# Kernel tuning notes

Measured on AMD Instinct MI355X. Metric: run time of the kernel, lower is better.

## Reference

```python
import jax, jax.numpy as jnp
import numpy as np

B, C, H, W = 4, 256, 64, 64
CQK = C // 8  # 32


def setup_inputs() -> dict:
    key = jax.random.key(0)
    ks = jax.random.split(key, 8)
    s = 0.05
    return {
        "x": jax.random.normal(ks[0], (B, C, H, W), dtype=jnp.float32),
        "wq": jax.random.normal(ks[1], (CQK, C), dtype=jnp.float32) * s,
        "bq": jax.random.normal(ks[2], (CQK,), dtype=jnp.float32) * s,
        "wk": jax.random.normal(ks[3], (CQK, C), dtype=jnp.float32) * s,
        "bk": jax.random.normal(ks[4], (CQK,), dtype=jnp.float32) * s,
        "wv": jax.random.normal(ks[5], (C, C), dtype=jnp.float32) * s,
        "bv": jax.random.normal(ks[6], (C,), dtype=jnp.float32) * s,
        "gamma": jax.random.normal(ks[7], (1,), dtype=jnp.float32),
    }


def reference(x, wq, bq, wk, bk, wv, bv, gamma):
    b, c, h, w = x.shape
    n = h * w
    xf = x.reshape(b, c, n)  # (B, C, N)
    # 1x1 conv + bias + ReLU (Conv2d wrapper default activate='relu')
    q = jax.nn.relu(jnp.einsum('oc,bcn->bon', wq, xf) + bq[:, None])  # (B, CQK, N)
    k = jax.nn.relu(jnp.einsum('oc,bcn->bon', wk, xf) + bk[:, None])  # (B, CQK, N)
    v = jax.nn.relu(jnp.einsum('oc,bcn->bon', wv, xf) + bv[:, None])  # (B, C, N)
    # energy[b, i, j] = sum_c q[b, c, i] * k[b, c, j]
    energy = jnp.einsum('bci,bcj->bij', q, k)  # (B, N, N)
    attention = jax.nn.softmax(energy, axis=-1)
    # out[b, c, i] = sum_j v[b, c, j] * attention[b, i, j]
    out = jnp.einsum('bcj,bij->bci', v, attention)  # (B, C, N)
    out = out.reshape(b, c, h, w)
    return gamma[0] * out + x
```

## Files before the change

### kernel.cpp

```cpp
#include <hip/hip_runtime.h>
#include <stdint.h>


#define NB 4
#define CD 256
#define ND 4096
#define CQ 32
#define LOG2E 1.4426950408889634f

typedef __attribute__((ext_vector_type(4))) float f32x4;
typedef __attribute__((ext_vector_type(8))) _Float16 f16x8;
typedef __attribute__((ext_vector_type(4))) unsigned short u16x4;
typedef __attribute__((ext_vector_type(8))) unsigned short u16x8;
typedef __attribute__((ext_vector_type(2))) unsigned int u32x2;
typedef __attribute__((ext_vector_type(4))) int i32x4;

static __device__ __forceinline__ unsigned short f2h(float f) {
    union { _Float16 h; unsigned short u; } cv; cv.h = (_Float16)f; return cv.u;
}
static __device__ __forceinline__ float fexp2(float xv) {
    float r; asm("v_exp_f32 %0, %1" : "=v"(r) : "v"(xv)); return r;
}

__global__ __launch_bounds__(256) void cvt_kernel(
    const float* __restrict__ x,
    const float* __restrict__ wq, const float* __restrict__ wk,
    const float* __restrict__ wv,
    unsigned short* __restrict__ xh, unsigned short* __restrict__ Wh)
{
    __shared__ unsigned short xt[64 * 72];
    if (blockIdx.x >= 1024) {
        const int idx = (blockIdx.x - 1024) * 256 + threadIdx.x;
        const int m = idx >> 6, kq = (idx & 63) << 2;
        const float* src = (m < 32) ? (wq + (size_t)m * CD + kq)
                         : (m < 64) ? (wk + (size_t)(m - 32) * CD + kq)
                                    : (wv + (size_t)(m - 64) * CD + kq);
        const f32x4 v = *reinterpret_cast<const f32x4*>(src);
        u16x4 h;
#pragma unroll
        for (int u = 0; u < 4; ++u) h[u] = f2h(v[u]);
        *reinterpret_cast<u16x4*>(Wh + (size_t)m * CD + kq) = h;
        return;
    }
    const int t  = threadIdx.x;
    const int nt = blockIdx.x & 63, ct = (blockIdx.x >> 6) & 3, b = blockIdx.x >> 8;
    const int n0 = nt << 6, c0 = ct << 6;

    const float* xb = x + ((size_t)(b * CD + c0)) * ND + n0;
#pragma unroll
    for (int s = t; s < 1024; s += 256) {
        const int c = s >> 4, nq = (s & 15) << 2;
        const f32x4 v = *reinterpret_cast<const f32x4*>(xb + (size_t)c * ND + nq);
        u16x4 h;
#pragma unroll
        for (int u = 0; u < 4; ++u) h[u] = f2h(v[u]);
        *reinterpret_cast<u16x4*>(&xt[c * 72 + nq]) = h;
    }
    __syncthreads();

    const int n = t >> 2, cb = (t & 3) << 4;
    u16x8 o0, o1;
#pragma unroll
    for (int u = 0; u < 8; ++u) o0[u] = xt[(cb + u) * 72 + n];
#pragma unroll
    for (int u = 0; u < 8; ++u) o1[u] = xt[(cb + 8 + u) * 72 + n];
    unsigned short* dst = xh + ((size_t)(b * ND + n0 + n)) * CD + c0 + cb;
    *reinterpret_cast<u16x8*>(dst)     = o0;
    *reinterpret_cast<u16x8*>(dst + 8) = o1;
}

__global__ __launch_bounds__(320) void proj_kernel(
    const unsigned short* __restrict__ Wh, const unsigned short* __restrict__ xh,
    const float* __restrict__ bq, const float* __restrict__ bk,
    const float* __restrict__ bv,
    unsigned short* __restrict__ Qt, unsigned short* __restrict__ Kt,
    unsigned short* __restrict__ Vp)
{
    const int tid = threadIdx.x;
    const int lane = tid & 63;
    const int w = __builtin_amdgcn_readfirstlane(tid >> 6);
    const int m16 = lane & 15, g4 = lane >> 4;
    const int b = blockIdx.x >> 6, n0 = (blockIdx.x & 63) << 6;

    f32x4 acc[4][4];
#pragma unroll
    for (int a = 0; a < 4; ++a)
#pragma unroll
        for (int c = 0; c < 4; ++c) acc[a][c] = (f32x4){0.f, 0.f, 0.f, 0.f};

    const unsigned short* Wrow = Wh + (size_t)(w * 64 + m16) * CD;
    const unsigned short* Xrow = xh + ((size_t)(b * ND + n0 + m16)) * CD;

#pragma unroll
    for (int ks = 0; ks < 8; ++ks) {
        const int ko = ks * 32 + g4 * 8;
        f16x8 af[4], bf[4];
#pragma unroll
        for (int ms = 0; ms < 4; ++ms)
            af[ms] = *reinterpret_cast<const f16x8*>(Wrow + (size_t)ms * 16 * CD + ko);
#pragma unroll
        for (int ns = 0; ns < 4; ++ns)
            bf[ns] = *reinterpret_cast<const f16x8*>(Xrow + (size_t)ns * 16 * CD + ko);
        if (w == 0) {
#pragma unroll
            for (int ms = 0; ms < 4; ++ms)
#pragma unroll
                for (int ns = 0; ns < 4; ++ns)
                    acc[ms][ns] = __builtin_amdgcn_mfma_f32_16x16x32_f16(
                        af[ms], bf[ns], acc[ms][ns], 0, 0, 0);
        } else {
#pragma unroll
            for (int ms = 0; ms < 4; ++ms)
#pragma unroll
                for (int ns = 0; ns < 4; ++ns)
                    acc[ms][ns] = __builtin_amdgcn_mfma_f32_16x16x32_f16(
                        bf[ns], af[ms], acc[ms][ns], 0, 0, 0);
        }
    }

    if (w == 0) {
#pragma unroll
        for (int ms = 0; ms < 4; ++ms) {
            const int seg = ms * 16;
            const int mb  = seg + g4 * 4;
            const f32x4 bias = (seg < 32) ? *reinterpret_cast<const f32x4*>(bq + mb)
                                          : *reinterpret_cast<const f32x4*>(bk + (mb - 32));
#pragma unroll
            for (int ns = 0; ns < 4; ++ns) {
                const int n = n0 + ns * 16 + m16;
                u16x4 h;
                if (seg < 32) {
#pragma unroll
                    for (int r = 0; r < 4; ++r)
                        h[r] = f2h(fmaxf(acc[ms][ns][r] + bias[r], 0.f) * LOG2E);
                    *reinterpret_cast<u16x4*>(Qt + ((size_t)(b * ND + n)) * CQ + mb) = h;
                } else {
#pragma unroll
                    for (int r = 0; r < 4; ++r)
                        h[r] = f2h(fmaxf(acc[ms][ns][r] + bias[r], 0.f));
                    *reinterpret_cast<u16x4*>(Kt + ((size_t)(b * ND + n)) * CQ + (mb - 32)) = h;
                }
            }
        }
    } else {
        const int cbase = (w - 1) * 64;
#pragma unroll
        for (int ms = 0; ms < 4; ++ms) {
            const int c = cbase + ms * 16 + m16;
            const float bval = bv[c];
#pragma unroll
            for (int ns = 0; ns < 4; ++ns) {
                const int n = n0 + ns * 16 + g4 * 4;
                u16x4 h;
#pragma unroll
                for (int r = 0; r < 4; ++r)
                    h[r] = f2h(fmaxf(acc[ms][ns][r] + bval, 0.f));
                unsigned short* dst = Vp
                    + ((size_t)((b * 128 + (n >> 5)) * 16 + (c >> 4))) * 512
                    + ((((n >> 3) & 3) * 16 + (c & 15)) * 8) + (n & 7);
                *reinterpret_cast<u16x4*>(dst) = h;
            }
        }
    }
}

__global__ __launch_bounds__(512, 2) void attn_kernel(
    const unsigned short* __restrict__ Qt, const unsigned short* __restrict__ Kt,
    const unsigned short* __restrict__ Vp, const float* __restrict__ x,
    const float* __restrict__ gamma, float* __restrict__ out)
{
    __shared__ __align__(16) unsigned char smem[68096];
    __shared__ int gctr[2];
    float* scales = reinterpret_cast<float*>(smem + 32768);
    int*   flags  = reinterpret_cast<int*>(smem + 34816);
    float* Ocomb  = reinterpret_cast<float*>(smem);
    float* mfin   = reinterpret_cast<float*>(smem + 66560);
    float* lfin   = reinterpret_cast<float*>(smem + 67072);
    float* wfac   = reinterpret_cast<float*>(smem + 67584);

    const int tid  = threadIdx.x;
    const int lane = tid & 63;
    const int w8   = __builtin_amdgcn_readfirstlane(tid >> 6);
    const int g    = w8 >> 2;
    const int ws   = w8 & 3;
    const int m16  = lane & 15;
    const int g4   = lane >> 4;
    const int wg   = (blockIdx.x & 7) * 32 + (blockIdx.x >> 3);
    const int b    = wg >> 6;
    const int i0   = (wg & 63) << 6;

    if (tid < 2) gctr[tid] = 0;
    __syncthreads();

    const f16x8 qfrag = *reinterpret_cast<const f16x8*>(
        Qt + ((size_t)(b * ND + i0 + ws * 16 + m16)) * CQ + g4 * 8);
    const unsigned short* kb = Kt + ((size_t)(b * ND + m16)) * CQ + g4 * 8;
    const unsigned short* vpc =
        Vp + ((size_t)(b * 128 * 16 + ws * 4)) * 512 + lane * 8;

    f32x4 oacc[4][4];
#pragma unroll
    for (int a = 0; a < 4; ++a)
#pragma unroll
        for (int c = 0; c < 4; ++c) oacc[a][c] = (f32x4){0.f, 0.f, 0.f, 0.f};
    float mrow = -1e30f;
    float lrow = 0.f;
    const f32x4 zero4 = {0.f, 0.f, 0.f, 0.f};

    const int jbase = g * 2048;
    const int irow  = ws * 16 + m16;
    const int iswz  = (m16 & 7) << 4;

    auto LOADK = [&](f16x8 (&kr)[4], int j) {
#pragma unroll
        for (int t = 0; t < 4; ++t)
            kr[t] = *reinterpret_cast<const f16x8*>(kb + (size_t)(j + t * 16) * CQ);
    };

    auto GSYNC = [&](int k) {
        asm volatile("s_waitcnt lgkmcnt(0)" ::: "memory");
        if (lane == 0) atomicAdd(&gctr[g], 1);
        const int tgt = (k + 1) * 4;
        int cv;
        do {
            __builtin_amdgcn_s_sleep(1);
            cv = __builtin_amdgcn_readfirstlane(*(volatile int*)&gctr[g]);
        } while (cv < tgt);
    };

    auto STEP = [&](int k, f16x8 (&kc)[4], f16x8 (&kn)[4]) {
        const int j0  = jbase + k * 64;
        const int par = k & 1;
        unsigned char* pb = smem + g * 16384 + par * 8192;

        const int jblk0 = j0 >> 5;
        f16x8 vf[2][4];
#pragma unroll
        for (int jh = 0; jh < 2; ++jh)
#pragma unroll
            for (int cs = 0; cs < 4; ++cs)
                vf[jh][cs] = *reinterpret_cast<const f16x8*>(
                    vpc + (size_t)((jblk0 + jh) * 16 + cs) * 512);
        const int jn = (k < 31) ? (j0 + 64) : jbase;
        LOADK(kn, jn);

        f32x4 s[4];
#pragma unroll
        for (int t = 0; t < 4; ++t)
            s[t] = __builtin_amdgcn_mfma_f32_16x16x32_f16(kc[t], qfrag, zero4, 0, 0, 0);

        float pm = s[0][0];
#pragma unroll
        for (int t = 0; t < 4; ++t)
#pragma unroll
            for (int r = 0; r < 4; ++r) pm = fmaxf(pm, s[t][r]);
        float sc = 1.0f;
        int myresc = 0;
        if (__ballot(pm <= mrow + 8.0f) != ~0ull) {
            float pr = fmaxf(pm, __shfl_xor(pm, 16));
            pr = fmaxf(pr, __shfl_xor(pr, 32));
            const float mnew = fmaxf(mrow, pr);
            sc = fexp2(mrow - mnew);
            mrow = mnew;
            myresc = 1;
        }
        float rs = 0.f;
#pragma unroll
        for (int t = 0; t < 4; ++t)
#pragma unroll
            for (int r = 0; r < 4; ++r) { s[t][r] = fexp2(s[t][r] - mrow); rs += s[t][r]; }
        lrow = lrow * sc + rs;

#pragma unroll
        for (int t = 0; t < 4; ++t) {
            u32x2 pw;
            pw[0] = __builtin_bit_cast(unsigned int,
                        __builtin_amdgcn_cvt_pkrtz(s[t][0], s[t][1]));
            pw[1] = __builtin_bit_cast(unsigned int,
                        __builtin_amdgcn_cvt_pkrtz(s[t][2], s[t][3]));
            const int lo = (irow * 128 + t * 32 + g4 * 8) ^ iswz;
            *reinterpret_cast<u32x2*>(pb + lo) = pw;
        }
        if (g4 == 0)   scales[(g * 2 + par) * 64 + irow] = sc;
        if (lane == 0) flags[(g * 2 + par) * 4 + ws] = myresc;

        GSYNC(k);

        const i32x4 fl = *reinterpret_cast<const i32x4*>(flags + (g * 2 + par) * 4);
        const int anyresc = __builtin_amdgcn_readfirstlane(fl[0] | fl[1] | fl[2] | fl[3]);
        if (anyresc) {
#pragma unroll
            for (int is = 0; is < 4; ++is) {
                const f32x4 sr = *reinterpret_cast<const f32x4*>(
                    scales + (g * 2 + par) * 64 + is * 16 + g4 * 4);
#pragma unroll
                for (int r = 0; r < 4; ++r)
#pragma unroll
                    for (int cs = 0; cs < 4; ++cs) oacc[is][cs][r] *= sr[r];
            }
        }

        __builtin_amdgcn_s_setprio(1);
#pragma unroll
        for (int jh = 0; jh < 2; ++jh) {
#pragma unroll
            for (int is = 0; is < 4; ++is) {
                const int lo = ((is * 16 + m16) * 128 + jh * 64 + g4 * 16) ^ iswz;
                const f16x8 pf = *reinterpret_cast<const f16x8*>(pb + lo);
#pragma unroll
                for (int cs = 0; cs < 4; ++cs)
                    oacc[is][cs] = __builtin_amdgcn_mfma_f32_16x16x32_f16(
                        pf, vf[jh][cs], oacc[is][cs], 0, 0, 0);
            }
        }
        __builtin_amdgcn_s_setprio(0);
    };

    f16x8 kA[4], kB[4];
    LOADK(kA, jbase);

#pragma unroll 1
    for (int k2 = 0; k2 < 16; ++k2) {
        STEP(2 * k2,     kA, kB);
        STEP(2 * k2 + 1, kB, kA);
    }

    lrow += __shfl_xor(lrow, 16);
    lrow += __shfl_xor(lrow, 32);
    if (g4 == 0) { mfin[g * 64 + irow] = mrow; lfin[g * 64 + irow] = lrow; }
    __syncthreads();

    if (tid < 128) {
        const int gg = tid >> 6, i = tid & 63;
        const float m0 = mfin[i], m1 = mfin[64 + i];
        const float M  = fmaxf(m0, m1);
        const float e0 = fexp2(m0 - M), e1 = fexp2(m1 - M);
        const float den = lfin[i] * e0 + lfin[64 + i] * e1;
        wfac[gg * 64 + i] = ((gg == 0) ? e0 : e1) / den;
    }
    __syncthreads();

    if (g == 0) {
#pragma unroll
        for (int is = 0; is < 4; ++is) {
            const f32x4 f = *reinterpret_cast<const f32x4*>(wfac + is * 16 + g4 * 4);
#pragma unroll
            for (int cs = 0; cs < 4; ++cs)
#pragma unroll
                for (int r = 0; r < 4; ++r)
                    Ocomb[(is * 16 + g4 * 4 + r) * 260 + ws * 64 + cs * 16 + m16] =
                        oacc[is][cs][r] * f[r];
        }
    }
    __syncthreads();
    if (g == 1) {
#pragma unroll
        for (int is = 0; is < 4; ++is) {
            const f32x4 f = *reinterpret_cast<const f32x4*>(wfac + 64 + is * 16 + g4 * 4);
#pragma unroll
            for (int cs = 0; cs < 4; ++cs)
#pragma unroll
                for (int r = 0; r < 4; ++r)
                    Ocomb[(is * 16 + g4 * 4 + r) * 260 + ws * 64 + cs * 16 + m16] +=
                        oacc[is][cs][r] * f[r];
        }
    }
    __syncthreads();

    const float gm = gamma[0];
#pragma unroll
    for (int pass = 0; pass < 8; ++pass) {
        const int c  = (tid >> 4) + pass * 32;
        const int ib = (tid & 15) * 4;
        f32x4 o;
#pragma unroll
        for (int u = 0; u < 4; ++u) o[u] = Ocomb[(ib + u) * 260 + c];
        const size_t idx = ((size_t)(b * CD + c)) * ND + i0 + ib;
        const f32x4 xv = *reinterpret_cast<const f32x4*>(x + idx);
        f32x4 res;
#pragma unroll
        for (int u = 0; u < 4; ++u) res[u] = gm * o[u] + xv[u];
        *reinterpret_cast<f32x4*>(out + idx) = res;
    }
}

extern "C" void kernel_launch(void* const* d_in, const int* in_sizes, int n_in,
                              void* d_out, int out_size, void* d_ws, size_t ws_size,
                              hipStream_t stream) {
    const float* x     = (const float*)d_in[0];
    const float* wq    = (const float*)d_in[1];
    const float* bq    = (const float*)d_in[2];
    const float* wk    = (const float*)d_in[3];
    const float* bk    = (const float*)d_in[4];
    const float* wv    = (const float*)d_in[5];
    const float* bv    = (const float*)d_in[6];
    const float* gamma = (const float*)d_in[7];

    unsigned short* Qt = (unsigned short*)d_ws;
    unsigned short* Kt = Qt + (size_t)NB * ND * CQ;
    unsigned short* Vp = Kt + (size_t)NB * ND * CQ;
    unsigned short* Wh = Vp + (size_t)NB * CD * ND;
    unsigned short* xh = Wh + (size_t)320 * CD;
    float* out = (float*)d_out;

    cvt_kernel<<<dim3(1104),     dim3(256), 0, stream>>>(x, wq, wk, wv, xh, Wh);
    proj_kernel<<<dim3(NB * 64), dim3(320), 0, stream>>>(Wh, xh, bq, bk, bv, Qt, Kt, Vp);
    attn_kernel<<<dim3(NB * 64), dim3(512), 0, stream>>>(Qt, Kt, Vp, x, gamma, out);
}
```

Before: 71.71 us.

## Fuse x fp16 conversion into projection and split attention keys across three wave groups

The x transpose/convert pass moves into proj_kernel, which loads fp32 x directly into swizzled LDS as fp16. This removes the xh round-trip through global memory and leaves a small weight-only conversion kernel. The attention kernel grows from 8 to 12 waves, split into three key-range groups of 22/21/21 chunks instead of two halves, merged with a three-way softmax rescale. This adds parallelism per block, but the larger block and changed launch bounds may cut occupancy and add one more serialized combine phase.

```diff
diff --git a/kernel.cpp b/kernel.cpp
--- a/kernel.cpp
+++ b/kernel.cpp
@@ -11,7 +11,6 @@
 typedef __attribute__((ext_vector_type(4))) float f32x4;
 typedef __attribute__((ext_vector_type(8))) _Float16 f16x8;
 typedef __attribute__((ext_vector_type(4))) unsigned short u16x4;
-typedef __attribute__((ext_vector_type(8))) unsigned short u16x8;
 typedef __attribute__((ext_vector_type(2))) unsigned int u32x2;
 typedef __attribute__((ext_vector_type(4))) int i32x4;
 
@@ -22,66 +21,53 @@
     float r; asm("v_exp_f32 %0, %1" : "=v"(r) : "v"(xv)); return r;
 }
 
-__global__ __launch_bounds__(256) void cvt_kernel(
-    const float* __restrict__ x,
+__global__ __launch_bounds__(256) void wcvt_kernel(
     const float* __restrict__ wq, const float* __restrict__ wk,
-    const float* __restrict__ wv,
-    unsigned short* __restrict__ xh, unsigned short* __restrict__ Wh)
+    const float* __restrict__ wv, unsigned short* __restrict__ Wh)
 {
-    __shared__ unsigned short xt[64 * 72];
-    if (blockIdx.x >= 1024) {
-        const int idx = (blockIdx.x - 1024) * 256 + threadIdx.x;
-        const int m = idx >> 6, kq = (idx & 63) << 2;
-        const float* src = (m < 32) ? (wq + (size_t)m * CD + kq)
-                         : (m < 64) ? (wk + (size_t)(m - 32) * CD + kq)
-                                    : (wv + (size_t)(m - 64) * CD + kq);
-        const f32x4 v = *reinterpret_cast<const f32x4*>(src);
-        u16x4 h;
-#pragma unroll
-        for (int u = 0; u < 4; ++u) h[u] = f2h(v[u]);
-        *reinterpret_cast<u16x4*>(Wh + (size_t)m * CD + kq) = h;
-        return;
-    }
-    const int t  = threadIdx.x;
-    const int nt = blockIdx.x & 63, ct = (blockIdx.x >> 6) & 3, b = blockIdx.x >> 8;
-    const int n0 = nt << 6, c0 = ct << 6;
-
-    const float* xb = x + ((size_t)(b * CD + c0)) * ND + n0;
-#pragma unroll
-    for (int s = t; s < 1024; s += 256) {
-        const int c = s >> 4, nq = (s & 15) << 2;
-        const f32x4 v = *reinterpret_cast<const f32x4*>(xb + (size_t)c * ND + nq);
-        u16x4 h;
-#pragma unroll
-        for (int u = 0; u < 4; ++u) h[u] = f2h(v[u]);
-        *reinterpret_cast<u16x4*>(&xt[c * 72 + nq]) = h;
-    }
-    __syncthreads();
-
-    const int n = t >> 2, cb = (t & 3) << 4;
-    u16x8 o0, o1;
-#pragma unroll
-    for (int u = 0; u < 8; ++u) o0[u] = xt[(cb + u) * 72 + n];
-#pragma unroll
-    for (int u = 0; u < 8; ++u) o1[u] = xt[(cb + 8 + u) * 72 + n];
-    unsigned short* dst = xh + ((size_t)(b * ND + n0 + n)) * CD + c0 + cb;
-    *reinterpret_cast<u16x8*>(dst)     = o0;
-    *reinterpret_cast<u16x8*>(dst + 8) = o1;
+    const int idx = blockIdx.x * 256 + threadIdx.x;
+    const int m = idx >> 6, kq = (idx & 63) << 2;
+    const float* src = (m < 32) ? (wq + (size_t)m * CD + kq)
+                     : (m < 64) ? (wk + (size_t)(m - 32) * CD + kq)
+                                : (wv + (size_t)(m - 64) * CD + kq);
+    const f32x4 v = *reinterpret_cast<const f32x4*>(src);
+    u16x4 h;
+#pragma unroll
+    for (int u = 0; u < 4; ++u) h[u] = f2h(v[u]);
+    *reinterpret_cast<u16x4*>(Wh + (size_t)m * CD + kq) = h;
 }
 
 __global__ __launch_bounds__(320) void proj_kernel(
-    const unsigned short* __restrict__ Wh, const unsigned short* __restrict__ xh,
+    const float* __restrict__ x, const unsigned short* __restrict__ Wh,
     const float* __restrict__ bq, const float* __restrict__ bk,
     const float* __restrict__ bv,
     unsigned short* __restrict__ Qt, unsigned short* __restrict__ Kt,
     unsigned short* __restrict__ Vp)
 {
+    __shared__ __align__(16) unsigned char xls[64 * 512];
+
     const int tid = threadIdx.x;
     const int lane = tid & 63;
     const int w = __builtin_amdgcn_readfirstlane(tid >> 6);
     const int m16 = lane & 15, g4 = lane >> 4;
     const int b = blockIdx.x >> 6, n0 = (blockIdx.x & 63) << 6;
 
+    {
+        const float* xb = x + (size_t)b * CD * ND + n0;
+#pragma unroll 1
+        for (int idx = tid; idx < 4096; idx += 320) {
+            const int c = idx >> 4, nq = (idx & 15) << 2;
+            const f32x4 v = *reinterpret_cast<const f32x4*>(xb + (size_t)c * ND + nq);
+#pragma unroll
+            for (int r = 0; r < 4; ++r) {
+                const int row = nq + r;
+                const int ad = (row * 512 + c * 2) ^ ((row & 7) << 4);
+                *reinterpret_cast<unsigned short*>(&xls[ad]) = f2h(v[r]);
+            }
+        }
+    }
+    __syncthreads();
+
     f32x4 acc[4][4];
 #pragma unroll
     for (int a = 0; a < 4; ++a)
@@ -89,7 +75,7 @@
         for (int c = 0; c < 4; ++c) acc[a][c] = (f32x4){0.f, 0.f, 0.f, 0.f};
 
     const unsigned short* Wrow = Wh + (size_t)(w * 64 + m16) * CD;
-    const unsigned short* Xrow = xh + ((size_t)(b * ND + n0 + m16)) * CD;
+    const int bswz = (m16 & 7) << 4;
 
 #pragma unroll
     for (int ks = 0; ks < 8; ++ks) {
@@ -99,8 +85,10 @@
         for (int ms = 0; ms < 4; ++ms)
             af[ms] = *reinterpret_cast<const f16x8*>(Wrow + (size_t)ms * 16 * CD + ko);
 #pragma unroll
-        for (int ns = 0; ns < 4; ++ns)
-            bf[ns] = *reinterpret_cast<const f16x8*>(Xrow + (size_t)ns * 16 * CD + ko);
+        for (int ns = 0; ns < 4; ++ns) {
+            const int ad = ((ns * 16 + m16) * 512 + ko * 2) ^ bswz;
+            bf[ns] = *reinterpret_cast<const f16x8*>(&xls[ad]);
+        }
         if (w == 0) {
 #pragma unroll
             for (int ms = 0; ms < 4; ++ms)
@@ -164,32 +152,32 @@
     }
 }
 
-__global__ __launch_bounds__(512, 2) void attn_kernel(
+__global__ __launch_bounds__(768) void attn_kernel(
     const unsigned short* __restrict__ Qt, const unsigned short* __restrict__ Kt,
     const unsigned short* __restrict__ Vp, const float* __restrict__ x,
     const float* __restrict__ gamma, float* __restrict__ out)
 {
-    __shared__ __align__(16) unsigned char smem[68096];
-    __shared__ int gctr[2];
-    float* scales = reinterpret_cast<float*>(smem + 32768);
-    int*   flags  = reinterpret_cast<int*>(smem + 34816);
+    __shared__ __align__(16) unsigned char smem[68864];
+    __shared__ int gctr[3];
+    float* scales = reinterpret_cast<float*>(smem + 49152);
+    int*   flags  = reinterpret_cast<int*>(smem + 50688);
     float* Ocomb  = reinterpret_cast<float*>(smem);
     float* mfin   = reinterpret_cast<float*>(smem + 66560);
-    float* lfin   = reinterpret_cast<float*>(smem + 67072);
-    float* wfac   = reinterpret_cast<float*>(smem + 67584);
+    float* lfin   = reinterpret_cast<float*>(smem + 67328);
+    float* wfac   = reinterpret_cast<float*>(smem + 68096);
 
     const int tid  = threadIdx.x;
     const int lane = tid & 63;
-    const int w8   = __builtin_amdgcn_readfirstlane(tid >> 6);
-    const int g    = w8 >> 2;
-    const int ws   = w8 & 3;
+    const int w12  = __builtin_amdgcn_readfirstlane(tid >> 6);
+    const int g    = (w12 >= 8) ? 2 : (w12 >> 2);
+    const int ws   = (w12 >= 8) ? (w12 - 8) : (w12 & 3);
     const int m16  = lane & 15;
     const int g4   = lane >> 4;
     const int wg   = (blockIdx.x & 7) * 32 + (blockIdx.x >> 3);
     const int b    = wg >> 6;
     const int i0   = (wg & 63) << 6;
 
-    if (tid < 2) gctr[tid] = 0;
+    if (tid < 3) gctr[tid] = 0;
     __syncthreads();
 
     const f16x8 qfrag = *reinterpret_cast<const f16x8*>(
@@ -207,9 +195,10 @@
     float lrow = 0.f;
     const f32x4 zero4 = {0.f, 0.f, 0.f, 0.f};
 
-    const int jbase = g * 2048;
-    const int irow  = ws * 16 + m16;
-    const int iswz  = (m16 & 7) << 4;
+    const int cbase  = (g == 0) ? 0 : (g == 1) ? 22 : 43;
+    const int nsteps = (g == 0) ? 22 : 21;
+    const int irow   = ws * 16 + m16;
+    const int iswz   = (m16 & 7) << 4;
 
     auto LOADK = [&](f16x8 (&kr)[4], int j) {
 #pragma unroll
@@ -217,10 +206,10 @@
             kr[t] = *reinterpret_cast<const f16x8*>(kb + (size_t)(j + t * 16) * CQ);
     };
 
-    auto GSYNC = [&](int k) {
+    auto GSYNC = [&](int s) {
         asm volatile("s_waitcnt lgkmcnt(0)" ::: "memory");
         if (lane == 0) atomicAdd(&gctr[g], 1);
-        const int tgt = (k + 1) * 4;
+        const int tgt = (s + 1) * 4;
         int cv;
         do {
             __builtin_amdgcn_s_sleep(1);
@@ -228,9 +217,9 @@
         } while (cv < tgt);
     };
 
-    auto STEP = [&](int k, f16x8 (&kc)[4], f16x8 (&kn)[4]) {
-        const int j0  = jbase + k * 64;
-        const int par = k & 1;
+    auto STEP = [&](int s, f16x8 (&kc)[4], f16x8 (&kn)[4]) {
+        const int j0  = (cbase + s) * 64;
+        const int par = s & 1;
         unsigned char* pb = smem + g * 16384 + par * 8192;
 
         const int jblk0 = j0 >> 5;
@@ -241,19 +230,19 @@
             for (int cs = 0; cs < 4; ++cs)
                 vf[jh][cs] = *reinterpret_cast<const f16x8*>(
                     vpc + (size_t)((jblk0 + jh) * 16 + cs) * 512);
-        const int jn = (k < 31) ? (j0 + 64) : jbase;
+        const int jn = (s + 1 < nsteps) ? (j0 + 64) : cbase * 64;
         LOADK(kn, jn);
 
-        f32x4 s[4];
+        f32x4 sv[4];
 #pragma unroll
         for (int t = 0; t < 4; ++t)
-            s[t] = __builtin_amdgcn_mfma_f32_16x16x32_f16(kc[t], qfrag, zero4, 0, 0, 0);
-
-        float pm = s[0][0];
+            sv[t] = __builtin_amdgcn_mfma_f32_16x16x32_f16(kc[t], qfrag, zero4, 0, 0, 0);
+
+        float pm = sv[0][0];
 #pragma unroll
         for (int t = 0; t < 4; ++t)
 #pragma unroll
-            for (int r = 0; r < 4; ++r) pm = fmaxf(pm, s[t][r]);
+            for (int r = 0; r < 4; ++r) pm = fmaxf(pm, sv[t][r]);
         float sc = 1.0f;
         int myresc = 0;
         if (__ballot(pm <= mrow + 8.0f) != ~0ull) {
@@ -268,23 +257,23 @@
 #pragma unroll
         for (int t = 0; t < 4; ++t)
 #pragma unroll
-            for (int r = 0; r < 4; ++r) { s[t][r] = fexp2(s[t][r] - mrow); rs += s[t][r]; }
+            for (int r = 0; r < 4; ++r) { sv[t][r] = fexp2(sv[t][r] - mrow); rs += sv[t][r]; }
         lrow = lrow * sc + rs;
 
 #pragma unroll
         for (int t = 0; t < 4; ++t) {
             u32x2 pw;
             pw[0] = __builtin_bit_cast(unsigned int,
-                        __builtin_amdgcn_cvt_pkrtz(s[t][0], s[t][1]));
+                        __builtin_amdgcn_cvt_pkrtz(sv[t][0], sv[t][1]));
             pw[1] = __builtin_bit_cast(unsigned int,
-                        __builtin_amdgcn_cvt_pkrtz(s[t][2], s[t][3]));
+                        __builtin_amdgcn_cvt_pkrtz(sv[t][2], sv[t][3]));
             const int lo = (irow * 128 + t * 32 + g4 * 8) ^ iswz;
             *reinterpret_cast<u32x2*>(pb + lo) = pw;
         }
         if (g4 == 0)   scales[(g * 2 + par) * 64 + irow] = sc;
         if (lane == 0) flags[(g * 2 + par) * 4 + ws] = myresc;
 
-        GSYNC(k);
+        GSYNC(s);
 
         const i32x4 fl = *reinterpret_cast<const i32x4*>(flags + (g * 2 + par) * 4);
         const int anyresc = __builtin_amdgcn_readfirstlane(fl[0] | fl[1] | fl[2] | fl[3]);
@@ -317,12 +306,15 @@
     };
 
     f16x8 kA[4], kB[4];
-    LOADK(kA, jbase);
+    LOADK(kA, cbase * 64);
 
 #pragma unroll 1
-    for (int k2 = 0; k2 < 16; ++k2) {
-        STEP(2 * k2,     kA, kB);
-        STEP(2 * k2 + 1, kB, kA);
+    for (int s2 = 0; s2 < 11; ++s2) {
+        const int s0 = 2 * s2, s1 = s0 + 1;
+        if (s0 >= nsteps) break;
+        STEP(s0, kA, kB);
+        if (s1 >= nsteps) break;
+        STEP(s1, kB, kA);
     }
 
     lrow += __shfl_xor(lrow, 16);
@@ -330,48 +322,42 @@
     if (g4 == 0) { mfin[g * 64 + irow] = mrow; lfin[g * 64 + irow] = lrow; }
     __syncthreads();
 
-    if (tid < 128) {
+    if (tid < 192) {
         const int gg = tid >> 6, i = tid & 63;
-        const float m0 = mfin[i], m1 = mfin[64 + i];
-        const float M  = fmaxf(m0, m1);
-        const float e0 = fexp2(m0 - M), e1 = fexp2(m1 - M);
-        const float den = lfin[i] * e0 + lfin[64 + i] * e1;
-        wfac[gg * 64 + i] = ((gg == 0) ? e0 : e1) / den;
+        const float m0 = mfin[i], m1 = mfin[64 + i], m2 = mfin[128 + i];
+        const float M  = fmaxf(fmaxf(m0, m1), m2);
+        const float e0 = fexp2(m0 - M), e1 = fexp2(m1 - M), e2 = fexp2(m2 - M);
+        const float den = lfin[i] * e0 + lfin[64 + i] * e1 + lfin[128 + i] * e2;
+        wfac[gg * 64 + i] = ((gg == 0) ? e0 : (gg == 1) ? e1 : e2) / den;
     }
     __syncthreads();
 
-    if (g == 0) {
-#pragma unroll
-        for (int is = 0; is < 4; ++is) {
-            const f32x4 f = *reinterpret_cast<const f32x4*>(wfac + is * 16 + g4 * 4);
-#pragma unroll
-            for (int cs = 0; cs < 4; ++cs)
-#pragma unroll
-                for (int r = 0; r < 4; ++r)
-                    Ocomb[(is * 16 + g4 * 4 + r) * 260 + ws * 64 + cs * 16 + m16] =
-                        oacc[is][cs][r] * f[r];
-        }
-    }
-    __syncthreads();
-    if (g == 1) {
-#pragma unroll
-        for (int is = 0; is < 4; ++is) {
-            const f32x4 f = *reinterpret_cast<const f32x4*>(wfac + 64 + is * 16 + g4 * 4);
-#pragma unroll
-            for (int cs = 0; cs < 4; ++cs)
-#pragma unroll
-                for (int r = 0; r < 4; ++r)
-                    Ocomb[(is * 16 + g4 * 4 + r) * 260 + ws * 64 + cs * 16 + m16] +=
-                        oacc[is][cs][r] * f[r];
-        }
-    }
-    __syncthreads();
+#pragma unroll
+    for (int gg = 0; gg < 3; ++gg) {
+        if (g == gg) {
+#pragma unroll
+            for (int is = 0; is < 4; ++is) {
+                const f32x4 f = *reinterpret_cast<const f32x4*>(
+                    wfac + g * 64 + is * 16 + g4 * 4);
+#pragma unroll
+                for (int cs = 0; cs < 4; ++cs)
+#pragma unroll
+                    for (int r = 0; r < 4; ++r) {
+                        const int i = is * 16 + g4 * 4 + r;
+                        const int c = ws * 64 + cs * 16 + m16;
+                        if (gg == 0) Ocomb[i * 260 + c]  = oacc[is][cs][r] * f[r];
+                        else         Ocomb[i * 260 + c] += oacc[is][cs][r] * f[r];
+                    }
+            }
+        }
+        __syncthreads();
+    }
 
     const float gm = gamma[0];
-#pragma unroll
-    for (int pass = 0; pass < 8; ++pass) {
-        const int c  = (tid >> 4) + pass * 32;
-        const int ib = (tid & 15) * 4;
+#pragma unroll 1
+    for (int q = tid; q < 4096; q += 768) {
+        const int c  = q >> 4;
+        const int ib = (q & 15) * 4;
         f32x4 o;
 #pragma unroll
         for (int u = 0; u < 4; ++u) o[u] = Ocomb[(ib + u) * 260 + c];
@@ -400,10 +386,9 @@
     unsigned short* Kt = Qt + (size_t)NB * ND * CQ;
     unsigned short* Vp = Kt + (size_t)NB * ND * CQ;
     unsigned short* Wh = Vp + (size_t)NB * CD * ND;
-    unsigned short* xh = Wh + (size_t)320 * CD;
     float* out = (float*)d_out;
 
-    cvt_kernel<<<dim3(1104),     dim3(256), 0, stream>>>(x, wq, wk, wv, xh, Wh);
-    proj_kernel<<<dim3(NB * 64), dim3(320), 0, stream>>>(Wh, xh, bq, bk, bv, Qt, Kt, Vp);
-    attn_kernel<<<dim3(NB * 64), dim3(512), 0, stream>>>(Qt, Kt, Vp, x, gamma, out);
-}
+    wcvt_kernel<<<dim3(80),      dim3(256), 0, stream>>>(wq, wk, wv, Wh);
+    proj_kernel<<<dim3(NB * 64), dim3(320), 0, stream>>>(x, Wh, bq, bk, bv, Qt, Kt, Vp);
+    attn_kernel<<<dim3(NB * 64), dim3(768), 0, stream>>>(Qt, Kt, Vp, x, gamma, out);
+}
```

Result: faster. 68.13 us (-5.0%).

## Split attention over key halves across blocks and fuse x conversion into projection

Applied to the files above, without the earlier changes.

The attention grid doubles to 512 blocks. Each block handles half of the key range, writes fp16 partial outputs plus per-row max and sum, and a new combine kernel merges the two halves and applies the gamma residual. The intent is to fill more of the CUs, since 256 blocks underuse the device. Separately, x is converted to fp16 directly into LDS inside the projection kernel, removing the standalone transpose/convert pass and its global round trip. In exchange it adds an extra kernel launch, global traffic for the partial outputs, and fp16 rounding of the partial results.

```diff
diff --git a/kernel.cpp b/kernel.cpp
--- a/kernel.cpp
+++ b/kernel.cpp
@@ -13,75 +13,66 @@
 typedef __attribute__((ext_vector_type(4))) unsigned short u16x4;
 typedef __attribute__((ext_vector_type(8))) unsigned short u16x8;
 typedef __attribute__((ext_vector_type(2))) unsigned int u32x2;
+typedef __attribute__((ext_vector_type(4))) unsigned int u32x4;
 typedef __attribute__((ext_vector_type(4))) int i32x4;
 
 static __device__ __forceinline__ unsigned short f2h(float f) {
     union { _Float16 h; unsigned short u; } cv; cv.h = (_Float16)f; return cv.u;
 }
+static __device__ __forceinline__ float h2f(unsigned short u) {
+    union { unsigned short u; _Float16 h; } cv; cv.u = u; return (float)cv.h;
+}
 static __device__ __forceinline__ float fexp2(float xv) {
     float r; asm("v_exp_f32 %0, %1" : "=v"(r) : "v"(xv)); return r;
 }
 
-__global__ __launch_bounds__(256) void cvt_kernel(
-    const float* __restrict__ x,
+__global__ __launch_bounds__(256) void wcvt_kernel(
     const float* __restrict__ wq, const float* __restrict__ wk,
-    const float* __restrict__ wv,
-    unsigned short* __restrict__ xh, unsigned short* __restrict__ Wh)
+    const float* __restrict__ wv, unsigned short* __restrict__ Wh)
 {
-    __shared__ unsigned short xt[64 * 72];
-    if (blockIdx.x >= 1024) {
-        const int idx = (blockIdx.x - 1024) * 256 + threadIdx.x;
-        const int m = idx >> 6, kq = (idx & 63) << 2;
-        const float* src = (m < 32) ? (wq + (size_t)m * CD + kq)
-                         : (m < 64) ? (wk + (size_t)(m - 32) * CD + kq)
-                                    : (wv + (size_t)(m - 64) * CD + kq);
-        const f32x4 v = *reinterpret_cast<const f32x4*>(src);
-        u16x4 h;
-#pragma unroll
-        for (int u = 0; u < 4; ++u) h[u] = f2h(v[u]);
-        *reinterpret_cast<u16x4*>(Wh + (size_t)m * CD + kq) = h;
-        return;
-    }
-    const int t  = threadIdx.x;
-    const int nt = blockIdx.x & 63, ct = (blockIdx.x >> 6) & 3, b = blockIdx.x >> 8;
-    const int n0 = nt << 6, c0 = ct << 6;
-
-    const float* xb = x + ((size_t)(b * CD + c0)) * ND + n0;
-#pragma unroll
-    for (int s = t; s < 1024; s += 256) {
-        const int c = s >> 4, nq = (s & 15) << 2;
-        const f32x4 v = *reinterpret_cast<const f32x4*>(xb + (size_t)c * ND + nq);
-        u16x4 h;
-#pragma unroll
-        for (int u = 0; u < 4; ++u) h[u] = f2h(v[u]);
-        *reinterpret_cast<u16x4*>(&xt[c * 72 + nq]) = h;
-    }
-    __syncthreads();
-
-    const int n = t >> 2, cb = (t & 3) << 4;
-    u16x8 o0, o1;
-#pragma unroll
-    for (int u = 0; u < 8; ++u) o0[u] = xt[(cb + u) * 72 + n];
-#pragma unroll
-    for (int u = 0; u < 8; ++u) o1[u] = xt[(cb + 8 + u) * 72 + n];
-    unsigned short* dst = xh + ((size_t)(b * ND + n0 + n)) * CD + c0 + cb;
-    *reinterpret_cast<u16x8*>(dst)     = o0;
-    *reinterpret_cast<u16x8*>(dst + 8) = o1;
+    const int idx = blockIdx.x * 256 + threadIdx.x;
+    const int m = idx >> 6, kq = (idx & 63) << 2;
+    const float* src = (m < 32) ? (wq + (size_t)m * CD + kq)
+                     : (m < 64) ? (wk + (size_t)(m - 32) * CD + kq)
+                                : (wv + (size_t)(m - 64) * CD + kq);
+    const f32x4 v = *reinterpret_cast<const f32x4*>(src);
+    u16x4 h;
+#pragma unroll
+    for (int u = 0; u < 4; ++u) h[u] = f2h(v[u]);
+    *reinterpret_cast<u16x4*>(Wh + (size_t)m * CD + kq) = h;
 }
 
 __global__ __launch_bounds__(320) void proj_kernel(
-    const unsigned short* __restrict__ Wh, const unsigned short* __restrict__ xh,
+    const float* __restrict__ x, const unsigned short* __restrict__ Wh,
     const float* __restrict__ bq, const float* __restrict__ bk,
     const float* __restrict__ bv,
     unsigned short* __restrict__ Qt, unsigned short* __restrict__ Kt,
     unsigned short* __restrict__ Vp)
 {
+    __shared__ __align__(16) unsigned char xls[64 * 512];
+
     const int tid = threadIdx.x;
     const int lane = tid & 63;
     const int w = __builtin_amdgcn_readfirstlane(tid >> 6);
     const int m16 = lane & 15, g4 = lane >> 4;
     const int b = blockIdx.x >> 6, n0 = (blockIdx.x & 63) << 6;
 
+    {
+        const float* xb = x + (size_t)b * CD * ND + n0;
+#pragma unroll 1
+        for (int idx = tid; idx < 4096; idx += 320) {
+            const int c = idx >> 4, nq = (idx & 15) << 2;
+            const f32x4 v = *reinterpret_cast<const f32x4*>(xb + (size_t)c * ND + nq);
+#pragma unroll
+            for (int r = 0; r < 4; ++r) {
+                const int row = nq + r;
+                const int ad = (row * 512 + c * 2) ^ ((row & 7) << 4);
+                *reinterpret_cast<unsigned short*>(&xls[ad]) = f2h(v[r]);
+            }
+        }
+    }
+    __syncthreads();
+
     f32x4 acc[4][4];
 #pragma unroll
     for (int a = 0; a < 4; ++a)
@@ -89,7 +80,7 @@
         for (int c = 0; c < 4; ++c) acc[a][c] = (f32x4){0.f, 0.f, 0.f, 0.f};
 
     const unsigned short* Wrow = Wh + (size_t)(w * 64 + m16) * CD;
-    const unsigned short* Xrow = xh + ((size_t)(b * ND + n0 + m16)) * CD;
+    const int bswz = (m16 & 7) << 4;
 
 #pragma unroll
     for (int ks = 0; ks < 8; ++ks) {
@@ -99,8 +90,10 @@
         for (int ms = 0; ms < 4; ++ms)
             af[ms] = *reinterpret_cast<const f16x8*>(Wrow + (size_t)ms * 16 * CD + ko);
 #pragma unroll
-        for (int ns = 0; ns < 4; ++ns)
-            bf[ns] = *reinterpret_cast<const f16x8*>(Xrow + (size_t)ns * 16 * CD + ko);
+        for (int ns = 0; ns < 4; ++ns) {
+            const int ad = ((ns * 16 + m16) * 512 + ko * 2) ^ bswz;
+            bf[ns] = *reinterpret_cast<const f16x8*>(&xls[ad]);
+        }
         if (w == 0) {
 #pragma unroll
             for (int ms = 0; ms < 4; ++ms)
@@ -164,10 +157,10 @@
     }
 }
 
-__global__ __launch_bounds__(512, 2) void attn_kernel(
+__global__ __launch_bounds__(512, 4) void attn_kernel(
     const unsigned short* __restrict__ Qt, const unsigned short* __restrict__ Kt,
-    const unsigned short* __restrict__ Vp, const float* __restrict__ x,
-    const float* __restrict__ gamma, float* __restrict__ out)
+    const unsigned short* __restrict__ Vp,
+    unsigned short* __restrict__ OpH, float* __restrict__ Mb, float* __restrict__ Lb)
 {
     __shared__ __align__(16) unsigned char smem[68096];
     __shared__ int gctr[2];
@@ -185,8 +178,9 @@
     const int ws   = w8 & 3;
     const int m16  = lane & 15;
     const int g4   = lane >> 4;
-    const int wg   = (blockIdx.x & 7) * 32 + (blockIdx.x >> 3);
-    const int b    = wg >> 6;
+    const int wg   = (blockIdx.x & 7) * 64 + (blockIdx.x >> 3);
+    const int jh   = wg >> 8;
+    const int b    = (wg >> 6) & 3;
     const int i0   = (wg & 63) << 6;
 
     if (tid < 2) gctr[tid] = 0;
@@ -207,7 +201,7 @@
     float lrow = 0.f;
     const f32x4 zero4 = {0.f, 0.f, 0.f, 0.f};
 
-    const int jbase = g * 2048;
+    const int jbase = jh * 2048 + g * 1024;
     const int irow  = ws * 16 + m16;
     const int iswz  = (m16 & 7) << 4;
 
@@ -221,11 +215,11 @@
         asm volatile("s_waitcnt lgkmcnt(0)" ::: "memory");
         if (lane == 0) atomicAdd(&gctr[g], 1);
         const int tgt = (k + 1) * 4;
-        int cv;
-        do {
+        int cv = __builtin_amdgcn_readfirstlane(*(volatile int*)&gctr[g]);
+        while (cv < tgt) {
             __builtin_amdgcn_s_sleep(1);
             cv = __builtin_amdgcn_readfirstlane(*(volatile int*)&gctr[g]);
-        } while (cv < tgt);
+        }
     };
 
     auto STEP = [&](int k, f16x8 (&kc)[4], f16x8 (&kn)[4]) {
@@ -236,24 +230,24 @@
         const int jblk0 = j0 >> 5;
         f16x8 vf[2][4];
 #pragma unroll
-        for (int jh = 0; jh < 2; ++jh)
+        for (int jhh = 0; jhh < 2; ++jhh)
 #pragma unroll
             for (int cs = 0; cs < 4; ++cs)
-                vf[jh][cs] = *reinterpret_cast<const f16x8*>(
-                    vpc + (size_t)((jblk0 + jh) * 16 + cs) * 512);
-        const int jn = (k < 31) ? (j0 + 64) : jbase;
+                vf[jhh][cs] = *reinterpret_cast<const f16x8*>(
+                    vpc + (size_t)((jblk0 + jhh) * 16 + cs) * 512);
+        const int jn = (k < 15) ? (j0 + 64) : jbase;
         LOADK(kn, jn);
 
-        f32x4 s[4];
+        f32x4 sv[4];
 #pragma unroll
         for (int t = 0; t < 4; ++t)
-            s[t] = __builtin_amdgcn_mfma_f32_16x16x32_f16(kc[t], qfrag, zero4, 0, 0, 0);
-
-        float pm = s[0][0];
+            sv[t] = __builtin_amdgcn_mfma_f32_16x16x32_f16(kc[t], qfrag, zero4, 0, 0, 0);
+
+        float pm = sv[0][0];
 #pragma unroll
         for (int t = 0; t < 4; ++t)
 #pragma unroll
-            for (int r = 0; r < 4; ++r) pm = fmaxf(pm, s[t][r]);
+            for (int r = 0; r < 4; ++r) pm = fmaxf(pm, sv[t][r]);
         float sc = 1.0f;
         int myresc = 0;
         if (__ballot(pm <= mrow + 8.0f) != ~0ull) {
@@ -268,16 +262,16 @@
 #pragma unroll
         for (int t = 0; t < 4; ++t)
 #pragma unroll
-            for (int r = 0; r < 4; ++r) { s[t][r] = fexp2(s[t][r] - mrow); rs += s[t][r]; }
+            for (int r = 0; r < 4; ++r) { sv[t][r] = fexp2(sv[t][r] - mrow); rs += sv[t][r]; }
         lrow = lrow * sc + rs;
 
 #pragma unroll
         for (int t = 0; t < 4; ++t) {
             u32x2 pw;
             pw[0] = __builtin_bit_cast(unsigned int,
-                        __builtin_amdgcn_cvt_pkrtz(s[t][0], s[t][1]));
+                        __builtin_amdgcn_cvt_pkrtz(sv[t][0], sv[t][1]));
             pw[1] = __builtin_bit_cast(unsigned int,
-                        __builtin_amdgcn_cvt_pkrtz(s[t][2], s[t][3]));
+                        __builtin_amdgcn_cvt_pkrtz(sv[t][2], sv[t][3]));
             const int lo = (irow * 128 + t * 32 + g4 * 8) ^ iswz;
             *reinterpret_cast<u32x2*>(pb + lo) = pw;
         }
@@ -302,15 +296,15 @@
 
         __builtin_amdgcn_s_setprio(1);
 #pragma unroll
-        for (int jh = 0; jh < 2; ++jh) {
+        for (int jhh = 0; jhh < 2; ++jhh) {
 #pragma unroll
             for (int is = 0; is < 4; ++is) {
-                const int lo = ((is * 16 + m16) * 128 + jh * 64 + g4 * 16) ^ iswz;
+                const int lo = ((is * 16 + m16) * 128 + jhh * 64 + g4 * 16) ^ iswz;
                 const f16x8 pf = *reinterpret_cast<const f16x8*>(pb + lo);
 #pragma unroll
                 for (int cs = 0; cs < 4; ++cs)
                     oacc[is][cs] = __builtin_amdgcn_mfma_f32_16x16x32_f16(
-                        pf, vf[jh][cs], oacc[is][cs], 0, 0, 0);
+                        pf, vf[jhh][cs], oacc[is][cs], 0, 0, 0);
             }
         }
         __builtin_amdgcn_s_setprio(0);
@@ -320,7 +314,7 @@
     LOADK(kA, jbase);
 
 #pragma unroll 1
-    for (int k2 = 0; k2 < 16; ++k2) {
+    for (int k2 = 0; k2 < 8; ++k2) {
         STEP(2 * k2,     kA, kB);
         STEP(2 * k2 + 1, kB, kA);
     }
@@ -334,9 +328,13 @@
         const int gg = tid >> 6, i = tid & 63;
         const float m0 = mfin[i], m1 = mfin[64 + i];
         const float M  = fmaxf(m0, m1);
-        const float e0 = fexp2(m0 - M), e1 = fexp2(m1 - M);
-        const float den = lfin[i] * e0 + lfin[64 + i] * e1;
-        wfac[gg * 64 + i] = ((gg == 0) ? e0 : e1) / den;
+        const float e  = fexp2(((gg == 0) ? m0 : m1) - M);
+        wfac[gg * 64 + i] = e;
+        if (gg == 0) {
+            const float e1 = fexp2(m1 - M);
+            Mb[(size_t)wg * 64 + i] = M;
+            Lb[(size_t)wg * 64 + i] = lfin[i] * fexp2(m0 - M) + lfin[64 + i] * e1;
+        }
     }
     __syncthreads();
 
@@ -367,20 +365,64 @@
     }
     __syncthreads();
 
+#pragma unroll
+    for (int pass = 0; pass < 4; ++pass) {
+        const int q = tid + pass * 512;
+        const int c = q >> 3, i8 = (q & 7) * 8;
+        u32x4 o;
+#pragma unroll
+        for (int u = 0; u < 4; ++u)
+            o[u] = __builtin_bit_cast(unsigned int,
+                       __builtin_amdgcn_cvt_pkrtz(Ocomb[(i8 + 2 * u) * 260 + c],
+                                                  Ocomb[(i8 + 2 * u + 1) * 260 + c]));
+        *reinterpret_cast<u32x4*>(OpH + ((size_t)wg * 256 + c) * 64 + i8) = o;
+    }
+}
+
+__global__ __launch_bounds__(256) void combine_kernel(
+    const unsigned short* __restrict__ OpH, const float* __restrict__ Mb,
+    const float* __restrict__ Lb, const float* __restrict__ x,
+    const float* __restrict__ gamma, float* __restrict__ out)
+{
+    __shared__ float w0[64], w1[64];
+    const int tid = threadIdx.x;
+    const int pb  = blockIdx.x;
+    const int b   = pb >> 6, istrip = pb & 63;
+    const int wg0 = pb, wg1 = 256 + pb;
+
+    if (tid < 64) {
+        const float m0 = Mb[(size_t)wg0 * 64 + tid], m1 = Mb[(size_t)wg1 * 64 + tid];
+        const float l0 = Lb[(size_t)wg0 * 64 + tid], l1 = Lb[(size_t)wg1 * 64 + tid];
+        const float M  = fmaxf(m0, m1);
+        const float e0 = fexp2(m0 - M), e1 = fexp2(m1 - M);
+        const float den = l0 * e0 + l1 * e1;
+        w0[tid] = e0 / den;
+        w1[tid] = e1 / den;
+    }
+    __syncthreads();
+
     const float gm = gamma[0];
-#pragma unroll
+#pragma unroll 1
     for (int pass = 0; pass < 8; ++pass) {
-        const int c  = (tid >> 4) + pass * 32;
-        const int ib = (tid & 15) * 4;
-        f32x4 o;
-#pragma unroll
-        for (int u = 0; u < 4; ++u) o[u] = Ocomb[(ib + u) * 260 + c];
-        const size_t idx = ((size_t)(b * CD + c)) * ND + i0 + ib;
-        const f32x4 xv = *reinterpret_cast<const f32x4*>(x + idx);
-        f32x4 res;
-#pragma unroll
-        for (int u = 0; u < 4; ++u) res[u] = gm * o[u] + xv[u];
-        *reinterpret_cast<f32x4*>(out + idx) = res;
+        const int q = tid + pass * 256;
+        const int c = q >> 3, i8 = (q & 7) * 8;
+        const u16x8 o0 = *reinterpret_cast<const u16x8*>(
+            OpH + ((size_t)wg0 * 256 + c) * 64 + i8);
+        const u16x8 o1 = *reinterpret_cast<const u16x8*>(
+            OpH + ((size_t)wg1 * 256 + c) * 64 + i8);
+        const size_t idx = ((size_t)(b * CD + c)) * ND + istrip * 64 + i8;
+        const f32x4 xa = *reinterpret_cast<const f32x4*>(x + idx);
+        const f32x4 xb2 = *reinterpret_cast<const f32x4*>(x + idx + 4);
+        f32x4 ra, rb;
+#pragma unroll
+        for (int u = 0; u < 4; ++u) {
+            const float v0 = h2f(o0[u]) * w0[i8 + u] + h2f(o1[u]) * w1[i8 + u];
+            const float v1 = h2f(o0[u + 4]) * w0[i8 + u + 4] + h2f(o1[u + 4]) * w1[i8 + u + 4];
+            ra[u] = gm * v0 + xa[u];
+            rb[u] = gm * v1 + xb2[u];
+        }
+        *reinterpret_cast<f32x4*>(out + idx)     = ra;
+        *reinterpret_cast<f32x4*>(out + idx + 4) = rb;
     }
 }
 
@@ -396,14 +438,17 @@
     const float* bv    = (const float*)d_in[6];
     const float* gamma = (const float*)d_in[7];
 
-    unsigned short* Qt = (unsigned short*)d_ws;
-    unsigned short* Kt = Qt + (size_t)NB * ND * CQ;
-    unsigned short* Vp = Kt + (size_t)NB * ND * CQ;
-    unsigned short* Wh = Vp + (size_t)NB * CD * ND;
-    unsigned short* xh = Wh + (size_t)320 * CD;
+    unsigned short* Qt  = (unsigned short*)d_ws;
+    unsigned short* Kt  = Qt + (size_t)NB * ND * CQ;
+    unsigned short* Vp  = Kt + (size_t)NB * ND * CQ;
+    unsigned short* Wh  = Vp + (size_t)NB * CD * ND;
+    unsigned short* OpH = Wh + (size_t)320 * CD;
+    float* Mb = (float*)(OpH + (size_t)512 * 256 * 64);
+    float* Lb = Mb + (size_t)512 * 64;
     float* out = (float*)d_out;
 
-    cvt_kernel<<<dim3(1104),     dim3(256), 0, stream>>>(x, wq, wk, wv, xh, Wh);
-    proj_kernel<<<dim3(NB * 64), dim3(320), 0, stream>>>(Wh, xh, bq, bk, bv, Qt, Kt, Vp);
-    attn_kernel<<<dim3(NB * 64), dim3(512), 0, stream>>>(Qt, Kt, Vp, x, gamma, out);
-}
+    wcvt_kernel<<<dim3(80),      dim3(256), 0, stream>>>(wq, wk, wv, Wh);
+    proj_kernel<<<dim3(NB * 64), dim3(320), 0, stream>>>(x, Wh, bq, bk, bv, Qt, Kt, Vp);
+    attn_kernel<<<dim3(512),     dim3(512), 0, stream>>>(Qt, Kt, Vp, OpH, Mb, Lb);
+    combine_kernel<<<dim3(256),  dim3(256), 0, stream>>>(OpH, Mb, Lb, x, gamma, out);
+}
```

Result: slower. 249.4 us (+247.7%).
